# Performance work log

Hardware: AMD Instinct MI355X
Metric: run time of the kernel (lower is better)

Reference implementation:

```python
import math
import jax, jax.numpy as jnp
import numpy as np

S, B, H, D = 2048, 1, 16, 128  # seq, batch, heads, head_dim (hard-coded in source)
COEFF = 1.0  # layer_num = 1
NORM_FACTOR = math.sqrt(2048 / 16) * COEFF  # sqrt(HIDDEN/NUM_HEADS) * coeff


def setup_inputs() -> dict:
    key = jax.random.key(0)
    k1, k2, k3, k4, k5 = jax.random.split(key, 5)
    query_layer = jax.random.normal(k1, (S, B, H, D), dtype=jnp.float32)
    key_layer = jax.random.normal(k2, (S, B, H, D), dtype=jnp.float32)
    value_layer = jax.random.normal(k3, (S, B, H, D), dtype=jnp.float32)
    # causal mask, True = masked (Megatron convention)
    attention_mask = jnp.triu(jnp.ones((S, S), dtype=bool), k=1)[None, None]
    # per-head SVD right-singular-vector matrices (orthonormal-ish; random here)
    svd_qk = jax.random.normal(k4, (H, D, D), dtype=jnp.float32) / math.sqrt(D)
    svd_v = jax.random.normal(k5, (H, D, D), dtype=jnp.float32) / math.sqrt(D)
    return {"query_layer": query_layer, "key_layer": key_layer,
            "value_layer": value_layer, "attention_mask": attention_mask,
            "svd_qk": svd_qk, "svd_v": svd_v}


def reference(query_layer, key_layer, value_layer, attention_mask, svd_qk, svd_v):
    # q/k/v: [S, 1, H, D] -> project each head through its SVD matrix
    q = jnp.einsum('shd,hde->hse', query_layer[:, 0], svd_qk)  # [H,S,D]
    k = jnp.einsum('shd,hde->hse', key_layer[:, 0], svd_qk)    # [H,S,D]
    # qk_drop = 0 -> h_mask zeroing of columns is a no-op (faithfully skipped)
    scores = jnp.einsum('hqe,hke->hqk', q, k) / NORM_FACTOR    # [H,S,S]
    mask = attention_mask[0, 0]                                 # [S,S] bool
    scores = jnp.where(mask, jnp.float32(-10000.0), scores)
    # FusedScaleMaskSoftmax: scale by coeff, re-mask, softmax
    scaled = jnp.where(mask, jnp.float32(-10000.0), scores * COEFF)
    probs = jax.nn.softmax(scaled, axis=-1)                     # [H,S,S]
    # attention dropout is identity in eval mode
    v = jnp.einsum('shd,hde->hse', value_layer[:, 0], svd_v)    # [H,S,D]
    # vlinear_drop = 0 -> column zeroing is a no-op
    ctx = jnp.einsum('hqk,hke->qhe', probs, v)                  # [S,H,D]
    return ctx.reshape(S, B, H * D)                             # [S,1,2048]
```

## Files before the change

### kernel.cpp

```cpp
#include <hip/hip_runtime.h>
#include <hip/hip_bf16.h>
#include <math.h>

#define S_LEN 2048
#define NHEAD 16
#define DHEAD 128

typedef __attribute__((ext_vector_type(8)))  _Float16 f16x8;
typedef __attribute__((ext_vector_type(4)))  _Float16 f16x4;
typedef __attribute__((ext_vector_type(4)))  float    f32x4;
typedef __attribute__((ext_vector_type(16))) float    f32x16;

__device__ __forceinline__ void permswap(unsigned &a, unsigned &b) {
    asm volatile("v_permlane32_swap_b32 %0, %1" : "+v"(a), "+v"(b));
}

typedef __attribute__((address_space(3))) unsigned int lds_u32;
typedef __attribute__((address_space(1))) const unsigned int glb_u32;
__device__ __forceinline__ void gload16(const void* g, void* l) {
    __builtin_amdgcn_global_load_lds((glb_u32*)g, (lds_u32*)l, 16, 0, 0);
}

__global__ __launch_bounds__(256) void transpose_w_kernel(
    const float* __restrict__ w_qk, const float* __restrict__ w_v,
    _Float16* __restrict__ wqk_t, _Float16* __restrict__ wv_t)
{
    __shared__ float tile[32][33];
    const int mat = blockIdx.z;
    const int h   = blockIdx.y;
    const int t0  = blockIdx.x;
    const int dt  = (t0 >> 2) * 32;
    const int et  = (t0 & 3) * 32;
    const float* src = (mat ? w_v : w_qk) + (size_t)h * DHEAD * DHEAD;
    _Float16*   dst = (mat ? wv_t : wqk_t) + (size_t)h * DHEAD * DHEAD;
    const int tx = threadIdx.x & 31, ty = threadIdx.x >> 5;
#pragma unroll
    for (int k = 0; k < 4; ++k)
        tile[ty + 8 * k][tx] = src[(size_t)(dt + ty + 8 * k) * DHEAD + et + tx];
    __syncthreads();
#pragma unroll
    for (int k = 0; k < 4; ++k)
        dst[(size_t)(et + ty + 8 * k) * DHEAD + dt + tx] = (_Float16)tile[tx][ty + 8 * k];
}

__global__ __launch_bounds__(256) void proj_kernel(
    const float* __restrict__ q_in, const float* __restrict__ k_in,
    const float* __restrict__ v_in,
    const _Float16* __restrict__ wqk_t, const _Float16* __restrict__ wv_t,
    _Float16* __restrict__ Qp, _Float16* __restrict__ Kp, _Float16* __restrict__ Vt)
{
    const int h   = blockIdx.x >> 5;
    const int rb  = blockIdx.x & 31;
    const int wv  = threadIdx.x >> 6;
    const int lane = threadIdx.x & 63;
    const int r16 = lane & 15;
    const int kg  = lane >> 4;
    const int s_base = rb * 64 + wv * 16;
    const int s_row  = s_base + r16;
    const float INV_NORM = 0.12752211758f;

    f16x8 aq[4], ak[4], av[4];
    {
        const float* qr = q_in + ((size_t)s_row * NHEAD + h) * DHEAD;
        const float* kr = k_in + ((size_t)s_row * NHEAD + h) * DHEAD;
        const float* vr = v_in + ((size_t)s_row * NHEAD + h) * DHEAD;
#pragma unroll
        for (int kb = 0; kb < 4; ++kb) {
            const int d0 = kb * 32 + kg * 8;
            const f32x4 q0 = *(const f32x4*)(qr + d0), q1 = *(const f32x4*)(qr + d0 + 4);
            const f32x4 k0 = *(const f32x4*)(kr + d0), k1 = *(const f32x4*)(kr + d0 + 4);
            const f32x4 v0 = *(const f32x4*)(vr + d0), v1 = *(const f32x4*)(vr + d0 + 4);
#pragma unroll
            for (int i = 0; i < 4; ++i) {
                aq[kb][i] = (_Float16)q0[i];  aq[kb][i + 4] = (_Float16)q1[i];
                ak[kb][i] = (_Float16)k0[i];  ak[kb][i + 4] = (_Float16)k1[i];
                av[kb][i] = (_Float16)v0[i];  av[kb][i + 4] = (_Float16)v1[i];
            }
        }
    }

    const _Float16* wq_h = wqk_t + (size_t)h * DHEAD * DHEAD;
    const _Float16* wv_h = wv_t  + (size_t)h * DHEAD * DHEAD;

#pragma unroll 2
    for (int cb = 0; cb < 8; ++cb) {
        f32x4 accq = {0.f, 0.f, 0.f, 0.f};
        f32x4 acck = {0.f, 0.f, 0.f, 0.f};
        f32x4 accv = {0.f, 0.f, 0.f, 0.f};
        const int c = cb * 16 + r16;
#pragma unroll
        for (int kb = 0; kb < 4; ++kb) {
            const f16x8 bqk = *(const f16x8*)(wq_h + (size_t)c * DHEAD + kb * 32 + kg * 8);
            const f16x8 bv  = *(const f16x8*)(wv_h + (size_t)c * DHEAD + kb * 32 + kg * 8);
            accq = __builtin_amdgcn_mfma_f32_16x16x32_f16(bqk, aq[kb], accq, 0, 0, 0);
            acck = __builtin_amdgcn_mfma_f32_16x16x32_f16(bqk, ak[kb], acck, 0, 0, 0);
            accv = __builtin_amdgcn_mfma_f32_16x16x32_f16(av[kb], bv,  accv, 0, 0, 0);
        }
        f16x4 qv, kv4;
#pragma unroll
        for (int jj = 0; jj < 4; ++jj) {
            qv[jj]  = (_Float16)(accq[jj] * INV_NORM);
            kv4[jj] = (_Float16)acck[jj];
        }
        *(f16x4*)(Qp + ((size_t)h * S_LEN + s_base + r16) * DHEAD + cb * 16 + kg * 4) = qv;
        *(f16x4*)(Kp + ((size_t)h * S_LEN + s_base + r16) * DHEAD + cb * 16 + kg * 4) = kv4;
        f16x4 vvv;
#pragma unroll
        for (int jj = 0; jj < 4; ++jj) vvv[jj] = (_Float16)accv[jj];
        *(f16x4*)(Vt + ((size_t)h * DHEAD + c) * S_LEN + s_base + kg * 4) = vvv;
    }
}

__device__ __forceinline__ void stage_k4(const _Float16* kbase, _Float16* kst,
                                         int w, int lane, int par, int inext,
                                         int jmax_lock) {
#pragma unroll
    for (int cidx = 0; cidx < 4; ++cidx) {
        const int c    = 4 * w + cidx;
        const int slot = c >> 3;
        const int cc   = c & 7;
        const int jn   = 4 * inext + slot;
        if (jn < jmax_lock) {
            const int A    = cc * 1024 + lane * 16;
            const int srcO = A ^ (((A >> 8) & 15) << 4);
            const char* g  = (const char*)kbase + (size_t)jn * 8192 + srcO;
            char*       l  = (char*)kst + (size_t)(slot * 2 + par) * 8192
                                        + cc * 1024;
            gload16(g, l);
        }
    }
}

__global__ __launch_bounds__(512, 2) void attn_kernel(
    const _Float16* __restrict__ Qp, const _Float16* __restrict__ Kp,
    const _Float16* __restrict__ Vt, float* __restrict__ out)
{
    __shared__ _Float16 Kst[8][4096];
    __shared__ _Float16 obuf[2][3][32][132];
    __shared__ float    mlbuf[2][3][2][32];

    const int h    = blockIdx.y;
    const int w    = threadIdx.x >> 6;
    const int lane = threadIdx.x & 63;
    const int q    = lane & 31;
    const int hi   = lane >> 5;

    const int role = w & 3;
    const int qsub = w >> 2;

    const _Float16* kbase = Kp + (size_t)h * S_LEN * DHEAD;
    const _Float16* vbase = Vt + (size_t)h * DHEAD * S_LEN;

    const int lqk = q * DHEAD + hi * 8;
    const int lv  = q * S_LEN + hi * 8;
    const int swq = (q & 15) << 4;

    for (int ph = 0; ph < 2; ++ph) {
        const int t     = ph ? blockIdx.x : (31 - blockIdx.x);
        const int q0w   = t * 64 + qsub * 32;
        const int jmax  = 2 * t + 1 + qsub;
        const int jlock = 2 * t + 2;
        const int I     = (jlock + 3) >> 2;
        const int q_abs = q0w + q;

        const _Float16* qbase = Qp + ((size_t)h * S_LEN + q0w) * DHEAD;
        f16x8 qf[8];
#pragma unroll
        for (int m = 0; m < 8; ++m)
            qf[m] = *(const f16x8*)(qbase + lqk + m * 16);

        f32x16 acc[4];
#pragma unroll
        for (int e = 0; e < 4; ++e)
#pragma unroll
            for (int i = 0; i < 16; ++i) acc[e][i] = 0.f;
        float m_run = -1e30f, l_run = 0.f;

        stage_k4(kbase, &Kst[0][0], w, lane, 0, 0, jlock);

        int p = 0;
        for (int it = 0; it < I; ++it, p ^= 1) {
            __syncthreads();

            const int j   = 4 * it + role;
            const bool act = (j < jmax);
            const int kv0 = j * 32;

            f16x8 vf[8];
            if (act) {
#pragma unroll
                for (int e = 0; e < 4; ++e) {
                    const _Float16* vp = vbase + (size_t)e * 32 * S_LEN + lv + kv0;
                    vf[2 * e]     = *(const f16x8*)(vp);
                    vf[2 * e + 1] = *(const f16x8*)(vp + 16);
                }
            }

            f16x8 kf[8];
            if (act) {
                const char* kt = (const char*)&Kst[role * 2 + p][0];
#pragma unroll
                for (int m = 0; m < 8; ++m) {
                    const int L = q * 256 + m * 32 + hi * 16;
                    kf[m] = *(const f16x8*)(kt + (L ^ swq));
                }
            }

            if (it + 1 < I)
                stage_k4(kbase, &Kst[0][0], w, lane, p ^ 1, it + 1, jlock);

            if (act) {
                f32x16 s0, s1;
#pragma unroll
                for (int i = 0; i < 16; ++i) { s0[i] = 0.f; s1[i] = 0.f; }
                __builtin_amdgcn_s_setprio(1);
#pragma unroll
                for (int m = 0; m < 8; m += 2) {
                    s0 = __builtin_amdgcn_mfma_f32_32x32x16_f16(kf[m],     qf[m],     s0, 0, 0, 0);
                    s1 = __builtin_amdgcn_mfma_f32_32x32x16_f16(kf[m + 1], qf[m + 1], s1, 0, 0, 0);
                }
                __builtin_amdgcn_s_setprio(0);

                f32x16 sv = s0 + s1;

                if (kv0 == q0w) {
#pragma unroll
                    for (int i = 0; i < 16; ++i) {
                        const int krel = (i & 3) + 8 * (i >> 2) + 4 * hi;
                        if (kv0 + krel > q_abs) sv[i] = -1e30f;
                    }
                }

                float t0 = fmaxf(sv[0], sv[1]),  t1 = fmaxf(sv[2], sv[3]);
                float t2 = fmaxf(sv[4], sv[5]),  t3 = fmaxf(sv[6], sv[7]);
                float t4 = fmaxf(sv[8], sv[9]),  t5 = fmaxf(sv[10], sv[11]);
                float t6 = fmaxf(sv[12], sv[13]), t7 = fmaxf(sv[14], sv[15]);
                t0 = fmaxf(t0, t1); t2 = fmaxf(t2, t3);
                t4 = fmaxf(t4, t5); t6 = fmaxf(t6, t7);
                float tm = fmaxf(fmaxf(t0, t2), fmaxf(t4, t6));
                tm = fmaxf(tm, __shfl_xor(tm, 32, 64));

                if (!__all(tm - m_run <= 8.0f)) {
                    const float mnew = fmaxf(m_run, tm);
                    const float corr = exp2f(m_run - mnew);
                    l_run *= corr;
#pragma unroll
                    for (int e = 0; e < 4; ++e)
#pragma unroll
                        for (int i = 0; i < 16; ++i) acc[e][i] *= corr;
                    m_run = mnew;
                }

#pragma unroll
                for (int i = 0; i < 16; ++i) sv[i] = exp2f(sv[i] - m_run);
                float r0 = (sv[0] + sv[1]) + (sv[2] + sv[3]);
                float r1 = (sv[4] + sv[5]) + (sv[6] + sv[7]);
                float r2 = (sv[8] + sv[9]) + (sv[10] + sv[11]);
                float r3 = (sv[12] + sv[13]) + (sv[14] + sv[15]);
                float rs = (r0 + r1) + (r2 + r3);

                unsigned u0 = __builtin_bit_cast(unsigned, __builtin_amdgcn_cvt_pkrtz(sv[0],  sv[1]));
                unsigned u1 = __builtin_bit_cast(unsigned, __builtin_amdgcn_cvt_pkrtz(sv[2],  sv[3]));
                unsigned u2 = __builtin_bit_cast(unsigned, __builtin_amdgcn_cvt_pkrtz(sv[4],  sv[5]));
                unsigned u3 = __builtin_bit_cast(unsigned, __builtin_amdgcn_cvt_pkrtz(sv[6],  sv[7]));
                unsigned u4 = __builtin_bit_cast(unsigned, __builtin_amdgcn_cvt_pkrtz(sv[8],  sv[9]));
                unsigned u5 = __builtin_bit_cast(unsigned, __builtin_amdgcn_cvt_pkrtz(sv[10], sv[11]));
                unsigned u6 = __builtin_bit_cast(unsigned, __builtin_amdgcn_cvt_pkrtz(sv[12], sv[13]));
                unsigned u7 = __builtin_bit_cast(unsigned, __builtin_amdgcn_cvt_pkrtz(sv[14], sv[15]));
                permswap(u0, u2); permswap(u1, u3);
                permswap(u4, u6); permswap(u5, u7);
                union uf8 { unsigned w[4]; f16x8 v; };
                uf8 p0; p0.w[0] = u0; p0.w[1] = u1; p0.w[2] = u2; p0.w[3] = u3;
                uf8 p1; p1.w[0] = u4; p1.w[1] = u5; p1.w[2] = u6; p1.w[3] = u7;

                __builtin_amdgcn_s_setprio(1);
#pragma unroll
                for (int e = 0; e < 4; ++e) {
                    acc[e] = __builtin_amdgcn_mfma_f32_32x32x16_f16(vf[2 * e],     p0.v, acc[e], 0, 0, 0);
                    acc[e] = __builtin_amdgcn_mfma_f32_32x32x16_f16(vf[2 * e + 1], p1.v, acc[e], 0, 0, 0);
                }
                __builtin_amdgcn_s_setprio(0);

                rs += __shfl_xor(rs, 32, 64);
                l_run += rs;
            }
        }

        if (role != 0) {
            if (hi == 0) {
                mlbuf[qsub][role - 1][0][q] = m_run;
                mlbuf[qsub][role - 1][1][q] = l_run;
            }
#pragma unroll
            for (int e = 0; e < 4; ++e)
#pragma unroll
                for (int i = 0; i < 16; ++i) {
                    const int erow = e * 32 + (i & 3) + 8 * (i >> 2) + 4 * hi;
                    obuf[qsub][role - 1][q][erow] = (_Float16)acc[e][i];
                }
        }
        __syncthreads();
        if (role == 0) {
            const float m1 = mlbuf[qsub][0][0][q], l1 = mlbuf[qsub][0][1][q];
            const float m2 = mlbuf[qsub][1][0][q], l2 = mlbuf[qsub][1][1][q];
            const float m3 = mlbuf[qsub][2][0][q], l3 = mlbuf[qsub][2][1][q];
            const float ms = fmaxf(fmaxf(m_run, m1), fmaxf(m2, m3));
            const float c0 = exp2f(m_run - ms);
            const float c1 = exp2f(m1 - ms);
            const float c2 = exp2f(m2 - ms);
            const float c3 = exp2f(m3 - ms);
            const float rinv = 1.0f / (l_run * c0 + l1 * c1 + l2 * c2 + l3 * c3);
            float* orow = out + (size_t)q_abs * (NHEAD * DHEAD) + h * DHEAD;
#pragma unroll
            for (int e = 0; e < 4; ++e) {
#pragma unroll
                for (int g = 0; g < 4; ++g) {
                    f32x4 vv;
#pragma unroll
                    for (int c = 0; c < 4; ++c) {
                        const int i = g * 4 + c;
                        const int erow = e * 32 + 8 * g + 4 * hi + c;
                        vv[c] = (acc[e][i] * c0
                                 + (float)obuf[qsub][0][q][erow] * c1
                                 + (float)obuf[qsub][1][q][erow] * c2
                                 + (float)obuf[qsub][2][q][erow] * c3) * rinv;
                    }
                    *(f32x4*)(orow + e * 32 + 8 * g + 4 * hi) = vv;
                }
            }
        }
    }
}

extern "C" void kernel_launch(void* const* d_in, const int* in_sizes, int n_in,
                              void* d_out, int out_size, void* d_ws, size_t ws_size,
                              hipStream_t stream) {
    const float* q_in = (const float*)d_in[0];
    const float* k_in = (const float*)d_in[1];
    const float* v_in = (const float*)d_in[2];
    const float* w_qk = (const float*)d_in[4];
    const float* w_v  = (const float*)d_in[5];
    float* out = (float*)d_out;

    const size_t mat_elems = (size_t)NHEAD * S_LEN * DHEAD;
    const size_t w_elems   = (size_t)NHEAD * DHEAD * DHEAD;
    _Float16* Qp   = (_Float16*)d_ws;
    _Float16* Kp   = Qp + mat_elems;
    _Float16* Vt   = Kp + mat_elems;
    _Float16* Wqkt = Vt + mat_elems;
    _Float16* Wvt  = Wqkt + w_elems;

    transpose_w_kernel<<<dim3(16, NHEAD, 2), dim3(256), 0, stream>>>(w_qk, w_v, Wqkt, Wvt);
    proj_kernel<<<dim3(NHEAD * 32), dim3(256), 0, stream>>>(q_in, k_in, v_in, Wqkt, Wvt, Qp, Kp, Vt);
    attn_kernel<<<dim3(16, NHEAD), dim3(512), 0, stream>>>(Qp, Kp, Vt, out);
}
```

Baseline: 87.90 us.

## Stage V tiles through LDS with async loads and serialize split-K merge

V tiles are now double-buffered into a new swizzled LDS buffer with async global-to-LDS loads alongside K, instead of each wave reading V directly from global memory into registers. To make room in LDS, the cross-wave merge of partial softmax results is serialized: one role at a time writes its partial output to a single shared buffer, which role 0 folds in. The goal is to hide V load latency behind compute. The cost is extra barriers in the epilogue and more LDS per block, which may lower occupancy below the two blocks per CU requested.

```diff
diff --git a/kernel.cpp b/kernel.cpp
--- a/kernel.cpp
+++ b/kernel.cpp
@@ -111,9 +111,10 @@
     }
 }
 
-__device__ __forceinline__ void stage_k4(const _Float16* kbase, _Float16* kst,
-                                         int w, int lane, int par, int inext,
-                                         int jmax_lock) {
+__device__ __forceinline__ void stage_kv4(const _Float16* kbase, const _Float16* vbase,
+                                          char* ksm, char* vsm,
+                                          int w, int lane, int par, int inext,
+                                          int jmax_lock) {
 #pragma unroll
     for (int cidx = 0; cidx < 4; ++cidx) {
         const int c    = 4 * w + cidx;
@@ -121,12 +122,23 @@
         const int cc   = c & 7;
         const int jn   = 4 * inext + slot;
         if (jn < jmax_lock) {
-            const int A    = cc * 1024 + lane * 16;
-            const int srcO = A ^ (((A >> 8) & 15) << 4);
-            const char* g  = (const char*)kbase + (size_t)jn * 8192 + srcO;
-            char*       l  = (char*)kst + (size_t)(slot * 2 + par) * 8192
-                                        + cc * 1024;
-            gload16(g, l);
+            {
+                const int A    = cc * 1024 + lane * 16;
+                const int srcO = A ^ (((A >> 8) & 15) << 4);
+                const char* g  = (const char*)kbase + (size_t)jn * 8192 + srcO;
+                char*       l  = ksm + (size_t)(slot * 2 + par) * 8192 + cc * 1024;
+                gload16(g, l);
+            }
+            {
+                const int A   = cc * 1024 + lane * 16;
+                const int B   = A ^ (((A >> 7) & 3) << 4);
+                const int row = B >> 6;
+                const int off = B & 63;
+                const char* g = (const char*)vbase + (size_t)row * (S_LEN * 2)
+                                                   + (size_t)jn * 64 + off;
+                char*       l = vsm + (size_t)(slot * 2 + par) * 8192 + cc * 1024;
+                gload16(g, l);
+            }
         }
     }
 }
@@ -136,8 +148,9 @@
     const _Float16* __restrict__ Vt, float* __restrict__ out)
 {
     __shared__ _Float16 Kst[8][4096];
-    __shared__ _Float16 obuf[2][3][32][132];
-    __shared__ float    mlbuf[2][3][2][32];
+    __shared__ _Float16 Vst[8][4096];
+    __shared__ _Float16 obuf[2][32][132];
+    __shared__ float    mlbuf[2][2][32];
 
     const int h    = blockIdx.y;
     const int w    = threadIdx.x >> 6;
@@ -152,8 +165,8 @@
     const _Float16* vbase = Vt + (size_t)h * DHEAD * S_LEN;
 
     const int lqk = q * DHEAD + hi * 8;
-    const int lv  = q * S_LEN + hi * 8;
     const int swq = (q & 15) << 4;
+    const int swv = ((q >> 1) & 3) << 4;
 
     for (int ph = 0; ph < 2; ++ph) {
         const int t     = ph ? blockIdx.x : (31 - blockIdx.x);
@@ -176,7 +189,7 @@
             for (int i = 0; i < 16; ++i) acc[e][i] = 0.f;
         float m_run = -1e30f, l_run = 0.f;
 
-        stage_k4(kbase, &Kst[0][0], w, lane, 0, 0, jlock);
+        stage_kv4(kbase, vbase, (char*)Kst, (char*)Vst, w, lane, 0, 0, jlock);
 
         int p = 0;
         for (int it = 0; it < I; ++it, p ^= 1) {
@@ -186,15 +199,9 @@
             const bool act = (j < jmax);
             const int kv0 = j * 32;
 
-            f16x8 vf[8];
-            if (act) {
-#pragma unroll
-                for (int e = 0; e < 4; ++e) {
-                    const _Float16* vp = vbase + (size_t)e * 32 * S_LEN + lv + kv0;
-                    vf[2 * e]     = *(const f16x8*)(vp);
-                    vf[2 * e + 1] = *(const f16x8*)(vp + 16);
-                }
-            }
+            if (it + 1 < I)
+                stage_kv4(kbase, vbase, (char*)Kst, (char*)Vst,
+                          w, lane, p ^ 1, it + 1, jlock);
 
             f16x8 kf[8];
             if (act) {
@@ -206,8 +213,19 @@
                 }
             }
 
-            if (it + 1 < I)
-                stage_k4(kbase, &Kst[0][0], w, lane, p ^ 1, it + 1, jlock);
+            f16x8 vf[8];
+            if (act) {
+                const char* vt = (const char*)&Vst[role * 2 + p][0];
+#pragma unroll
+                for (int e = 0; e < 4; ++e) {
+#pragma unroll
+                    for (int half = 0; half < 2; ++half) {
+                        const int vrow = e * 32 + q;
+                        const int off  = (half * 32 + hi * 16) ^ swv;
+                        vf[2 * e + half] = *(const f16x8*)(vt + vrow * 64 + off);
+                    }
+                }
+            }
 
             if (act) {
                 f32x16 s0, s1;
@@ -286,30 +304,41 @@
             }
         }
 
-        if (role != 0) {
-            if (hi == 0) {
-                mlbuf[qsub][role - 1][0][q] = m_run;
-                mlbuf[qsub][role - 1][1][q] = l_run;
-            }
-#pragma unroll
-            for (int e = 0; e < 4; ++e)
-#pragma unroll
-                for (int i = 0; i < 16; ++i) {
-                    const int erow = e * 32 + (i & 3) + 8 * (i >> 2) + 4 * hi;
-                    obuf[qsub][role - 1][q][erow] = (_Float16)acc[e][i];
-                }
-        }
+        float mc = m_run, lc = l_run;
         __syncthreads();
+#pragma unroll
+        for (int r = 1; r <= 3; ++r) {
+            if (role == r) {
+                if (hi == 0) { mlbuf[qsub][0][q] = m_run; mlbuf[qsub][1][q] = l_run; }
+#pragma unroll
+                for (int e = 0; e < 4; ++e)
+#pragma unroll
+                    for (int i = 0; i < 16; ++i) {
+                        const int erow = e * 32 + (i & 3) + 8 * (i >> 2) + 4 * hi;
+                        obuf[qsub][q][erow] = (_Float16)acc[e][i];
+                    }
+            }
+            __syncthreads();
+            if (role == 0) {
+                const float mb = mlbuf[qsub][0][q];
+                const float lb = mlbuf[qsub][1][q];
+                const float ms = fmaxf(mc, mb);
+                const float ca = exp2f(mc - ms);
+                const float cb = exp2f(mb - ms);
+#pragma unroll
+                for (int e = 0; e < 4; ++e)
+#pragma unroll
+                    for (int i = 0; i < 16; ++i) {
+                        const int erow = e * 32 + (i & 3) + 8 * (i >> 2) + 4 * hi;
+                        acc[e][i] = acc[e][i] * ca + (float)obuf[qsub][q][erow] * cb;
+                    }
+                lc = lc * ca + lb * cb;
+                mc = ms;
+            }
+            __syncthreads();
+        }
         if (role == 0) {
-            const float m1 = mlbuf[qsub][0][0][q], l1 = mlbuf[qsub][0][1][q];
-            const float m2 = mlbuf[qsub][1][0][q], l2 = mlbuf[qsub][1][1][q];
-            const float m3 = mlbuf[qsub][2][0][q], l3 = mlbuf[qsub][2][1][q];
-            const float ms = fmaxf(fmaxf(m_run, m1), fmaxf(m2, m3));
-            const float c0 = exp2f(m_run - ms);
-            const float c1 = exp2f(m1 - ms);
-            const float c2 = exp2f(m2 - ms);
-            const float c3 = exp2f(m3 - ms);
-            const float rinv = 1.0f / (l_run * c0 + l1 * c1 + l2 * c2 + l3 * c3);
+            const float rinv = 1.0f / lc;
             float* orow = out + (size_t)q_abs * (NHEAD * DHEAD) + h * DHEAD;
 #pragma unroll
             for (int e = 0; e < 4; ++e) {
@@ -317,18 +346,13 @@
                 for (int g = 0; g < 4; ++g) {
                     f32x4 vv;
 #pragma unroll
-                    for (int c = 0; c < 4; ++c) {
-                        const int i = g * 4 + c;
-                        const int erow = e * 32 + 8 * g + 4 * hi + c;
-                        vv[c] = (acc[e][i] * c0
-                                 + (float)obuf[qsub][0][q][erow] * c1
-                                 + (float)obuf[qsub][1][q][erow] * c2
-                                 + (float)obuf[qsub][2][q][erow] * c3) * rinv;
-                    }
+                    for (int c = 0; c < 4; ++c)
+                        vv[c] = acc[e][g * 4 + c] * rinv;
                     *(f32x4*)(orow + e * 32 + 8 * g + 4 * hi) = vv;
                 }
             }
         }
+        __syncthreads();
     }
 }
 
```

Measured after the change: 96.89 us. 10.2% more time.
